# Optimization experiments

Measured on AMD Instinct MI355X. Metric: run time of the kernel, lower is better.

Reference implementation:

```python
import jax, jax.numpy as jnp
import numpy as np

MAP_X = 72; MAP_Y = 72      # global map grid
R = 300                      # number of rooms
MAXS = 8                     # rooms padded to 8x8 (zero-padded occupancy)
E = 32                       # room_embedding_width
N = 128                      # batch
CONV_CH = [64, 128, 256]; KS = [5, 3, 3]
FC = [512, 256]; OUT_W = 512


def setup_inputs() -> dict:
    key = jax.random.key(0)
    ks = jax.random.split(key, 20)
    rng = np.random.default_rng(0)
    widths = rng.integers(1, MAXS + 1, R)
    heights = rng.integers(1, MAXS + 1, R)
    # room_maps[i] is room.map transposed -> [width, height], zero-padded to [MAXS, MAXS]
    rm = np.zeros((R, MAXS, MAXS), np.int32)
    for i in range(R):
        rm[i, :widths[i], :heights[i]] = rng.integers(0, 2, (int(widths[i]), int(heights[i])))
    inp = {}
    # room top-left positions; rooms fit since max size is MAXS
    inp["X"] = jax.random.randint(ks[0], (N, R, 2), 0, MAP_X - MAXS + 1, dtype=jnp.int32)
    inp["room_maps"] = jnp.asarray(rm)
    inp["room_emb"] = jax.random.normal(ks[1], (R, E), jnp.float32)
    cin = [1 + E] + CONV_CH
    for i in range(3):
        k = KS[i]; fan = cin[i] * k * k
        inp[f"conv_w{i}"] = jax.random.normal(ks[2 + 2 * i], (cin[i + 1], cin[i], k, k), jnp.float32) / np.sqrt(fan).astype(np.float32)
        inp[f"conv_b{i}"] = jnp.zeros((cin[i + 1],), jnp.float32)
    fcd = [CONV_CH[-1]] + FC + [OUT_W]
    for i in range(3):
        inp[f"fc_w{i}"] = jax.random.normal(ks[10 + 2 * i], (fcd[i + 1], fcd[i]), jnp.float32) / np.sqrt(fcd[i]).astype(np.float32)
        inp[f"fc_b{i}"] = jnp.zeros((fcd[i + 1],), jnp.float32)
    return inp


def _encode_map(X, room_maps, room_emb):
    # Fused scatter: occupancy channel + embedding channels scattered in one pass.
    rm = room_maps.astype(room_emb.dtype)                    # [R, W, H]
    vals = jnp.concatenate(
        [rm[..., None], rm[..., None] * room_emb[:, None, None, :]], axis=-1
    )                                                        # [R, W, H, 1+E]
    ax = jnp.arange(MAXS)

    def one(pos):  # pos: [R, 2] positions for one batch element
        ix = jnp.broadcast_to(pos[:, 0, None, None] + ax[None, :, None], (R, MAXS, MAXS))
        iy = jnp.broadcast_to(pos[:, 1, None, None] + ax[None, None, :], (R, MAXS, MAXS))
        grid = jnp.zeros((MAP_X, MAP_Y, 1 + E), vals.dtype)
        # padded cells are zero so dropped/duplicate adds are exact
        return grid.at[ix, iy].add(vals, mode="drop")

    out = jax.vmap(one)(X)                                   # [N, MAP_X, MAP_Y, 1+E]
    # torch: transpose(1,3) -> [N, 1+E, MAP_Y, MAP_X]
    return jnp.transpose(out, (0, 3, 2, 1))


def _conv_relu(x, w, b, k):
    p = k // 2
    y = jax.lax.conv_general_dilated(
        x, w, (1, 1), [(p, p), (p, p)], dimension_numbers=("NCHW", "OIHW", "NCHW"))
    return jax.nn.relu(y + b[None, :, None, None])


def _maxpool3s2(x):
    return jax.lax.reduce_window(x, -jnp.inf, jax.lax.max, (1, 1, 3, 3), (1, 1, 2, 2), "VALID")


def reference(X, room_maps, room_emb, conv_w0, conv_b0, conv_w1, conv_b1, conv_w2, conv_b2, fc_w0, fc_b0, fc_w1, fc_b1, fc_w2, fc_b2):
    x = _encode_map(X, room_maps, room_emb)
    for w, b, k in ((conv_w0, conv_b0, KS[0]), (conv_w1, conv_b1, KS[1]), (conv_w2, conv_b2, KS[2])):
        x = _maxpool3s2(_conv_relu(x, w, b, k))
    x = jnp.mean(x, axis=(2, 3))                             # GlobalAvgPool2d
    x = jax.nn.relu(x @ fc_w0.T + fc_b0)
    x = jax.nn.relu(x @ fc_w1.T + fc_b1)
    return x @ fc_w2.T + fc_b2
```

## Files before the change

kernel.cpp:

```cpp
#include <hip/hip_runtime.h>
#include <hip/hip_bf16.h>
#include <cstdint>
#include <cstddef>

#define NB      128
#define RR      300
#define EMB     32

typedef __bf16 bf16x8 __attribute__((ext_vector_type(8)));
typedef float  f32x4  __attribute__((ext_vector_type(4)));
typedef unsigned short ushort8 __attribute__((ext_vector_type(8)));

__device__ __forceinline__ unsigned short f2bf(float f) {
    union { __hip_bfloat16 h; unsigned short u; } c;
    c.h = __float2bfloat16(f);
    return c.u;
}
__device__ __forceinline__ float bf2f(unsigned short u) {
    union { __hip_bfloat16 h; unsigned short u; } c;
    c.u = u;
    return __bfloat162float(c.h);
}

__device__ __forceinline__ void wpack_body(
    const float* __restrict__ w, unsigned short* __restrict__ wPT,
    int COUT, int CIN, int KK, int gpc, int idx, int total)
{
    if (idx >= total) return;
    int kk = idx & 31;
    int t  = idx >> 5;
    int oc = t % COUT;
    int kb = t / COUT;
    int g  = kb * 4 + (kk >> 3);
    int j  = kk & 7;
    int shift = g / gpc;
    int ci    = (g % gpc) * 8 + j;
    float v = (shift < KK && ci < CIN)
        ? w[(size_t)oc * CIN * KK + (size_t)ci * KK + shift] : 0.0f;
    wPT[idx] = f2bf(v);
}

__device__ __forceinline__ void fcT_body(
    const float* __restrict__ w, float* __restrict__ wT, int O, int I, int idx)
{
    if (idx >= O * I) return;
    int i = idx % I, o = idx / I;
    wT[(size_t)i * O + o] = w[idx];
}

__global__ __launch_bounds__(256) void prep_k(
    const int* __restrict__ rm, unsigned long long* __restrict__ masks,
    const float* __restrict__ cw0, unsigned short* __restrict__ WP0,
    const float* __restrict__ cw1, unsigned short* __restrict__ WP1,
    const float* __restrict__ cw2, unsigned short* __restrict__ WP2,
    int* __restrict__ kt0, int* __restrict__ kt1, int* __restrict__ kt2,
    const float* __restrict__ fw0, float* __restrict__ W0T,
    const float* __restrict__ fw1, float* __restrict__ W1T,
    const float* __restrict__ fw2, float* __restrict__ W2T)
{
    const int b = blockIdx.x;
    const int t = threadIdx.x;
    if (b < 2) {
        int r = b * 256 + t;
        if (r < RR) {
            unsigned long long m = 0ull;
            #pragma unroll
            for (int k = 0; k < 64; ++k)
                if (rm[r * 64 + k]) m |= (1ull << k);
            masks[r] = m;
        }
    } else if (b < 258) {
        wpack_body(cw0, WP0, 64, 33, 25, 5, (b - 2) * 256 + t, 32 * 64 * 32);
    } else if (b < 546) {
        wpack_body(cw1, WP1, 128, 64, 9, 8, (b - 258) * 256 + t, 18 * 128 * 32);
    } else if (b < 1698) {
        wpack_body(cw2, WP2, 256, 128, 9, 16, (b - 546) * 256 + t, 36 * 256 * 32);
    } else if (b < 1699) {
        #pragma unroll
        for (int which = 0; which < 3; ++which) {
            int ngr, gpc, K, Wp, CL;
            int* dst;
            if (which == 0)      { ngr = 128; gpc = 5;  K = 5; Wp = 20; CL = 40;  dst = kt0; }
            else if (which == 1) { ngr = 72;  gpc = 8;  K = 3; Wp = 37; CL = 72;  dst = kt1; }
            else                 { ngr = 144; gpc = 16; K = 3; Wp = 19; CL = 136; dst = kt2; }
            if (t < ngr) {
                int shift = t / gpc;
                int off = 0;
                if (shift < K * K) {
                    int ky = shift / K, kx = shift % K;
                    off = (ky * Wp + kx) * CL + (t % gpc) * 8;
                }
                dst[t] = off;
            }
        }
    } else if (b < 2211) {
        fcT_body(fw0, W0T, 512, 256, (b - 1699) * 256 + t);
    } else if (b < 2723) {
        fcT_body(fw1, W1T, 256, 512, (b - 2211) * 256 + t);
    } else {
        fcT_body(fw2, W2T, 512, 256, (b - 2723) * 256 + t);
    }
}

__device__ __forceinline__ void border_body(
    unsigned short* __restrict__ base, int Hp, int Wp, int CPG, int pad,
    int sampleStride, int nborder, int idx, int total)
{
    if (idx >= total) return;
    int c8 = idx % CPG;
    int t  = idx / CPG;
    int bi = t % nborder;
    int nl = t / nborder;

    int topN = pad * Wp;
    int y, x;
    if (bi < topN) {
        y = bi / Wp; x = bi - y * Wp;
    } else if (bi < 2 * topN) {
        int b2 = bi - topN;
        y = Hp - pad + b2 / Wp; x = b2 % Wp;
    } else {
        int mid = bi - 2 * topN;
        int rowlen = 2 * pad;
        y = pad + mid / rowlen;
        int r = mid % rowlen;
        x = r < pad ? r : Wp - pad + (r - pad);
    }
    uint4 z = make_uint4(0, 0, 0, 0);
    *reinterpret_cast<uint4*>(
        &base[((size_t)nl * sampleStride) +
              ((size_t)y * Wp + x) * (CPG * 8) + c8 * 8]) = z;
}

__global__ __launch_bounds__(256) void border2_k(
    unsigned short* __restrict__ bufC, int C_SS, int nb1, int Bc)
{
    int b = blockIdx.x;
    int t = threadIdx.x;
    if (b < nb1) {
        border_body(bufC, 37, 37, 8, 1, C_SS, 144, b * 256 + t, Bc * 144 * 8);
    } else {
        border_body(bufC + 87616, 19, 19, 16, 1, C_SS, 72,
                    (b - nb1) * 256 + t, Bc * 72 * 16);
    }
}

__global__ __launch_bounds__(512) void encode_k(
    const int* __restrict__ X, const unsigned long long* __restrict__ masks,
    const float* __restrict__ emb, unsigned short* __restrict__ G,
    int n0, int sampleStride)
{
    __shared__ float tile[4][72][33];
    __shared__ unsigned s_pos[RR];
    __shared__ unsigned long long s_mask[RR];
    __shared__ unsigned short s_list[320];
    __shared__ float s_emb[64 * 33];
    __shared__ int s_woff[8];
    __shared__ int s_cnt;

    const int nl = blockIdx.x, band = blockIdx.y;
    const int by = band * 4;
    const int n  = n0 + nl;
    const int tid = threadIdx.x;

    float* tf = &tile[0][0][0];
    for (int i = tid; i < 4 * 72 * 33; i += 512) tf[i] = 0.0f;

    const int2* Xp = reinterpret_cast<const int2*>(X);
    bool hot = false;
    if (tid < RR) {
        int2 pos = Xp[n * RR + tid];
        s_pos[tid]  = (unsigned)pos.x | ((unsigned)pos.y << 16);
        s_mask[tid] = masks[tid];
        hot = (pos.y <= by + 3) && (pos.y + 7 >= by);
    }
    unsigned long long bal = __ballot(hot);
    if ((tid & 63) == 0) s_woff[tid >> 6] = (int)__popcll(bal);
    __syncthreads();
    if (tid == 0) {
        int acc = 0;
        #pragma unroll
        for (int w = 0; w < 8; ++w) { int c = s_woff[w]; s_woff[w] = acc; acc += c; }
        s_cnt = acc;
    }
    __syncthreads();
    if (hot) {
        int w = tid >> 6, b = tid & 63;
        unsigned long long before = (b == 0) ? 0ull : (bal & ((1ull << b) - 1ull));
        s_list[s_woff[w] + (int)__popcll(before)] = (unsigned short)tid;
    }
    __syncthreads();

    const int lane = tid & 63;
    const int wvi  = tid >> 6;
    const int dx   = lane >> 3;
    const int c0   = (lane & 7) * 5;
    const int cnt  = s_cnt;

    for (int base = 0; base < cnt; base += 64) {
        int cn = cnt - base; if (cn > 64) cn = 64;
        for (int i = tid; i < cn * 33; i += 512) {
            int hi = i / 33, cc = i - hi * 33;
            int r = s_list[base + hi];
            s_emb[i] = (cc == 0) ? 1.0f : emb[r * EMB + cc - 1];
        }
        __syncthreads();

        int j = wvi;
        for (; j + 8 < cn; j += 16) {
            int rA = s_list[base + j];
            int rB = s_list[base + j + 8];
            unsigned pA = s_pos[rA], pB = s_pos[rB];
            unsigned long long mA = s_mask[rA] >> (dx * 8);
            unsigned long long mB = s_mask[rB] >> (dx * 8);
            int xA = (pA & 0xffff) + dx, yA = pA >> 16;
            int xB = (pB & 0xffff) + dx, yB = pB >> 16;
            float eA[5], eB[5];
            #pragma unroll
            for (int q = 0; q < 5; ++q) {
                eA[q] = (c0 + q < 33) ? s_emb[j * 33 + c0 + q] : 0.0f;
                eB[q] = (c0 + q < 33) ? s_emb[(j + 8) * 33 + c0 + q] : 0.0f;
            }
            #pragma unroll
            for (int dyb = 0; dyb < 4; ++dyb) {
                int dA = by + dyb - yA;
                if ((unsigned)dA < 8u && ((mA >> dA) & 1ull)) {
                    #pragma unroll
                    for (int q = 0; q < 5; ++q)
                        if (c0 + q < 33)
                            atomicAdd(&tile[dyb][xA][c0 + q], eA[q]);
                }
                int dB = by + dyb - yB;
                if ((unsigned)dB < 8u && ((mB >> dB) & 1ull)) {
                    #pragma unroll
                    for (int q = 0; q < 5; ++q)
                        if (c0 + q < 33)
                            atomicAdd(&tile[dyb][xB][c0 + q], eB[q]);
                }
            }
        }
        for (; j < cn; j += 8) {
            int r = s_list[base + j];
            unsigned pxy = s_pos[r];
            int px = pxy & 0xffff, py = pxy >> 16;
            unsigned long long mm = s_mask[r] >> (dx * 8);
            int x = px + dx;
            float ev[5];
            #pragma unroll
            for (int q = 0; q < 5; ++q)
                ev[q] = (c0 + q < 33) ? s_emb[j * 33 + c0 + q] : 0.0f;
            #pragma unroll
            for (int dyb = 0; dyb < 4; ++dyb) {
                int dyr = by + dyb - py;
                if ((unsigned)dyr < 8u && ((mm >> dyr) & 1ull)) {
                    #pragma unroll
                    for (int q = 0; q < 5; ++q)
                        if (c0 + q < 33)
                            atomicAdd(&tile[dyb][x][c0 + q], ev[q]);
                }
            }
        }
        __syncthreads();
    }
    __syncthreads();

    unsigned short* Gn = G + (size_t)nl * sampleStride;
    for (int i = tid; i < 4 * 72 * 10; i += 512) {
        int cc = i % 10;
        int t  = i / 10;
        int x  = t % 72;
        int dyb = t / 72;
        int c0w = cc * 4;
        unsigned short r[4];
        #pragma unroll
        for (int j = 0; j < 4; ++j)
            r[j] = (c0w + j < 33) ? f2bf(tile[dyb][x][c0w + j]) : 0;
        uint2 pk;
        pk.x = (unsigned)r[0] | ((unsigned)r[1] << 16);
        pk.y = (unsigned)r[2] | ((unsigned)r[3] << 16);
        *reinterpret_cast<uint2*>(
            &Gn[((size_t)(by + dyb + 2) * 76 + (x + 2)) * 40 + c0w]) = pk;
    }

    uint2 zz; zz.x = 0; zz.y = 0;
    for (int i = tid; i < 160; i += 512) {
        int cc = i % 10;
        int t  = i / 10;
        int ci = t & 3;
        int dyb = t >> 2;
        int x = ci < 2 ? ci : 72 + ci;
        *reinterpret_cast<uint2*>(
            &Gn[((size_t)(by + dyb + 2) * 76 + x) * 40 + cc * 4]) = zz;
    }
    if (band == 0 || band == 17) {
        int rbase = band == 0 ? 0 : 74;
        for (int i = tid; i < 2 * 76 * 10; i += 512) {
            int cc = i % 10;
            int t  = i / 10;
            int x  = t % 76;
            int r  = t / 76;
            *reinterpret_cast<uint2*>(
                &Gn[((size_t)(rbase + r) * 76 + x) * 40 + cc * 4]) = zz;
        }
    }
}

template<int KSTEPS>
__global__ __launch_bounds__(256, 3) void conv0_tile_k(
    const unsigned short* __restrict__ inP,
    const unsigned short* __restrict__ wPT,
    const int* __restrict__ ktab,
    const float* __restrict__ bias,
    unsigned short* __restrict__ out,
    int inSS, int outSS)
{
    constexpr int CL = 40;
    constexpr int LP = 72;
    __shared__ __align__(16) unsigned short slab[28 * 20 * CL];
    __shared__ int s_kt[KSTEPS * 4];
    unsigned short* s_c = slab;

    const int tid = threadIdx.x;
    const int tl  = blockIdx.x;
    const int nl  = blockIdx.y;
    const int tyi = tl / 5, txi = tl % 5;
    const int y0 = tyi * 24;
    const int x0 = txi < 4 ? txi * 16 : 56;

    const int lane = tid & 63, wv = tid >> 6, frow = lane & 15, fq = lane >> 4;

    if (tid < KSTEPS * 4) s_kt[tid] = ktab[tid];

    const unsigned short* in_n = inP + (size_t)nl * inSS;
    {
        const uint4* src = reinterpret_cast<const uint4*>(in_n);
        uint4* dst = reinterpret_cast<uint4*>(slab);
        #pragma unroll
        for (int it = 0; it < 11; ++it) {
            int q = tid + it * 256;
            if (q < 2800) {
                int r = q / 100, c = q - r * 100;
                dst[q] = src[((y0 + r) * 76 + x0) * 5 + c];
            }
        }
    }

    int ldsb[6];
    #pragma unroll
    for (int mf = 0; mf < 6; ++mf)
        ldsb[mf] = ((mf * 4 + wv) * 20 + frow) * CL;

    const unsigned short* wbase = wPT + (size_t)frow * 32 + fq * 8;

    f32x4 acc[6][4];
    #pragma unroll
    for (int a = 0; a < 6; ++a)
        #pragma unroll
        for (int b = 0; b < 4; ++b) acc[a][b] = (f32x4){0.f, 0.f, 0.f, 0.f};

    __syncthreads();

    #pragma unroll 2
    for (int kb = 0; kb < KSTEPS; ++kb) {
        int go = s_kt[kb * 4 + fq];
        bf16x8 af[6];
        #pragma unroll
        for (int mf = 0; mf < 6; ++mf)
            af[mf] = *reinterpret_cast<const bf16x8*>(&slab[ldsb[mf] + go]);
        const unsigned short* wk = wbase + (size_t)kb * 64 * 32;
        #pragma unroll
        for (int ng = 0; ng < 4; ++ng) {
            bf16x8 bf = *reinterpret_cast<const bf16x8*>(wk + ng * 16 * 32);
            #pragma unroll
            for (int mf = 0; mf < 6; ++mf)
                acc[mf][ng] = __builtin_amdgcn_mfma_f32_16x16x32_bf16(
                    af[mf], bf, acc[mf][ng], 0, 0, 0);
        }
    }

    unsigned short* out_n = out + (size_t)nl * outSS;
    const int erow = tid >> 2, eseg = tid & 3;
    #pragma unroll
    for (int mf = 0; mf < 6; ++mf) {
        __syncthreads();
        #pragma unroll
        for (int ng = 0; ng < 4; ++ng) {
            float bv = bias[ng * 16 + frow];
            #pragma unroll
            for (int j = 0; j < 4; ++j)
                s_c[(wv * 16 + fq * 4 + j) * LP + ng * 16 + frow] =
                    f2bf(fmaxf(acc[mf][ng][j] + bv, 0.0f));
        }
        __syncthreads();
        {
            int ty = mf * 4 + (erow >> 4);
            int tx = erow & 15;
            int pos = (y0 + ty) * 72 + (x0 + tx);
            ushort8 v0 = *reinterpret_cast<const ushort8*>(
                &s_c[erow * LP + eseg * 16]);
            ushort8 v1 = *reinterpret_cast<const ushort8*>(
                &s_c[erow * LP + eseg * 16 + 8]);
            unsigned short* op = out_n + (size_t)pos * 64 + eseg * 16;
            *reinterpret_cast<ushort8*>(op) = v0;
            *reinterpret_cast<ushort8*>(op + 8) = v1;
        }
    }
}

template<int MFRAG, int NG, int KH, int CPG, int CL, int SLAB, int KSTEPS>
__global__ __launch_bounds__(256, 2) void conv_mfma_k(
    const unsigned short* __restrict__ inP,
    const unsigned short* __restrict__ wPT,
    const int* __restrict__ ktab,
    const float* __restrict__ bias,
    unsigned short* __restrict__ out,
    int W, int Wp, int Mtot, int inSS, int outSS, int COUT)
{
    constexpr int Mblk = MFRAG * 64;
    constexpr int NOC  = NG * 16;
    constexpr int SEGS = NOC / 16;
    constexpr int LP   = NOC + 8;
    constexpr int CP   = CPG * 8;
    constexpr int SMEM = (SLAB * 2 > 64 * LP * 2) ? SLAB * 2 : 64 * LP * 2;
    __shared__ __align__(16) char smem[SMEM];
    __shared__ int s_kt[KSTEPS * 4];
    unsigned short* slab = reinterpret_cast<unsigned short*>(smem);
    unsigned short* s_c  = reinterpret_cast<unsigned short*>(smem);

    const int tid  = threadIdx.x;
    const int mb   = blockIdx.x;
    const int ocb  = blockIdx.y;
    const int nl   = blockIdx.z;
    const int lane = tid & 63;
    const int wv   = tid >> 6;
    const int frow = lane & 15;
    const int fq   = lane >> 4;

    if (tid < KSTEPS * 4) s_kt[tid] = ktab[tid];

    const int p0    = mb * Mblk;
    const int y0    = p0 / W;
    const int plast = (p0 + Mblk < Mtot ? p0 + Mblk : Mtot) - 1;
    const int rows  = plast / W - y0 + KH;

    const unsigned short* in_n =
        inP + (size_t)nl * inSS + (size_t)y0 * Wp * CP;
    const int nchunks = rows * Wp * CPG;
    for (int q = tid; q < nchunks; q += 256) {
        int pix = q / CPG, c8 = q - pix * CPG;
        uint4 v = reinterpret_cast<const uint4*>(in_n)[q];
        *reinterpret_cast<uint4*>(&slab[pix * CL + c8 * 8]) = v;
    }

    int ldsb[MFRAG];
    #pragma unroll
    for (int mf = 0; mf < MFRAG; ++mf) {
        int p  = p0 + mf * 64 + wv * 16 + frow;
        int pc = p < Mtot ? p : (Mtot - 1);
        int y  = pc / W;
        int x  = pc - y * W;
        ldsb[mf] = ((y - y0) * Wp + x) * CL;
    }
    const unsigned short* wbase =
        wPT + ((size_t)(ocb * NOC + frow)) * 32 + fq * 8;

    f32x4 acc[MFRAG][NG];
    #pragma unroll
    for (int mf = 0; mf < MFRAG; ++mf)
        #pragma unroll
        for (int ng = 0; ng < NG; ++ng)
            acc[mf][ng] = (f32x4){0.f, 0.f, 0.f, 0.f};

    __syncthreads();

    for (int kb = 0; kb < KSTEPS; ++kb) {
        int go = s_kt[kb * 4 + fq];
        bf16x8 af[MFRAG];
        #pragma unroll
        for (int mf = 0; mf < MFRAG; ++mf)
            af[mf] = *reinterpret_cast<const bf16x8*>(&slab[ldsb[mf] + go]);
        const unsigned short* wk = wbase + (size_t)kb * COUT * 32;
        #pragma unroll
        for (int ng = 0; ng < NG; ++ng) {
            bf16x8 bf = *reinterpret_cast<const bf16x8*>(wk + ng * 16 * 32);
            #pragma unroll
            for (int mf = 0; mf < MFRAG; ++mf)
                acc[mf][ng] = __builtin_amdgcn_mfma_f32_16x16x32_bf16(
                    af[mf], bf, acc[mf][ng], 0, 0, 0);
        }
    }

    unsigned short* out_n = out + (size_t)nl * outSS;
    #pragma unroll
    for (int mf = 0; mf < MFRAG; ++mf) {
        __syncthreads();
        #pragma unroll
        for (int ng = 0; ng < NG; ++ng) {
            float bv = bias[ocb * NOC + ng * 16 + frow];
            #pragma unroll
            for (int j = 0; j < 4; ++j)
                s_c[(wv * 16 + fq * 4 + j) * LP + ng * 16 + frow] =
                    f2bf(fmaxf(acc[mf][ng][j] + bv, 0.0f));
        }
        __syncthreads();
        for (int t = tid; t < 64 * SEGS; t += 256) {
            int row = t / SEGS, seg = t % SEGS;
            int p = p0 + mf * 64 + row;
            if (p < Mtot) {
                ushort8 v0 = *reinterpret_cast<const ushort8*>(
                    &s_c[row * LP + seg * 16]);
                ushort8 v1 = *reinterpret_cast<const ushort8*>(
                    &s_c[row * LP + seg * 16 + 8]);
                unsigned short* op =
                    out_n + (size_t)p * COUT + ocb * NOC + seg * 16;
                *reinterpret_cast<ushort8*>(op) = v0;
                *reinterpret_cast<ushort8*>(op + 8) = v1;
            }
        }
    }
}

__global__ __launch_bounds__(256) void pool_k(
    const unsigned short* __restrict__ in, unsigned short* __restrict__ out,
    int CG, int C, int W, int inSS,
    int HO, int WO, int Wpo, int outSS, int total)
{
    int idx = blockIdx.x * 256 + threadIdx.x;
    if (idx >= total) return;
    int cg = idx % CG;
    int t  = idx / CG;
    int x  = t % WO;
    t /= WO;
    int y  = t % HO;
    int nl = t / HO;

    const unsigned short* pin = in + (size_t)nl * inSS + cg * 8;
    ushort8 mx = {0,0,0,0,0,0,0,0};
    #pragma unroll
    for (int dy = 0; dy < 3; ++dy)
        #pragma unroll
        for (int dx = 0; dx < 3; ++dx) {
            ushort8 v = *reinterpret_cast<const ushort8*>(
                pin + ((size_t)(2 * y + dy) * W + (2 * x + dx)) * C);
            #pragma unroll
            for (int j = 0; j < 8; ++j) mx[j] = v[j] > mx[j] ? v[j] : mx[j];
        }
    *reinterpret_cast<ushort8*>(
        out + (size_t)nl * outSS +
        ((size_t)(y + 1) * Wpo + (x + 1)) * C + cg * 8) = mx;
}

__global__ __launch_bounds__(256) void pool2gap_k(
    const unsigned short* __restrict__ in, float* __restrict__ out,
    int inSS, int n0)
{
    __shared__ float red[4][4][8];
    const int nl = blockIdx.x;
    const int cg = blockIdx.y;
    const int tid = threadIdx.x;
    const int w  = tid >> 2;
    const int cq = tid & 3;
    const int y = w >> 3, x = w & 7;

    const unsigned short* p = in + (size_t)nl * inSS + cg * 32 + cq * 8;
    ushort8 mx = {0,0,0,0,0,0,0,0};
    #pragma unroll
    for (int dy = 0; dy < 3; ++dy)
        #pragma unroll
        for (int dx = 0; dx < 3; ++dx) {
            ushort8 v = *reinterpret_cast<const ushort8*>(
                p + ((size_t)(2 * y + dy) * 17 + (2 * x + dx)) * 256);
            #pragma unroll
            for (int j = 0; j < 8; ++j) mx[j] = v[j] > mx[j] ? v[j] : mx[j];
        }
    float s[8];
    #pragma unroll
    for (int j = 0; j < 8; ++j) s[j] = bf2f(mx[j]);
    #pragma unroll
    for (int m = 4; m < 64; m <<= 1)
        #pragma unroll
        for (int j = 0; j < 8; ++j)
            s[j] += __shfl_xor(s[j], m);
    if ((tid & 63) < 4) {
        #pragma unroll
        for (int j = 0; j < 8; ++j) red[tid >> 6][tid & 3][j] = s[j];
    }
    __syncthreads();
    if (tid < 32) {
        int cq2 = tid >> 3, j = tid & 7;
        float t = red[0][cq2][j] + red[1][cq2][j] + red[2][cq2][j] + red[3][cq2][j];
        out[(size_t)(n0 + nl) * 256 + cg * 32 + cq2 * 8 + j] = t * (1.0f / 64.0f);
    }
}

__global__ __launch_bounds__(256) void fc_fused_k(
    const float* __restrict__ in,
    const float* __restrict__ w0T, const float* __restrict__ b0,
    const float* __restrict__ w1T, const float* __restrict__ b1,
    const float* __restrict__ w2T, const float* __restrict__ b2,
    float* __restrict__ out)
{
    __shared__ float s_in[256], s_h0[512], s_h1[256];
    const int n = blockIdx.x, t = threadIdx.x;
    s_in[t] = in[(size_t)n * 256 + t];
    __syncthreads();
    float a0 = 0.f, a1 = 0.f;
    for (int i = 0; i < 256; ++i) {
        float v = s_in[i];
        a0 += v * w0T[i * 512 + t];
        a1 += v * w0T[i * 512 + t + 256];
    }
    s_h0[t]       = fmaxf(a0 + b0[t], 0.0f);
    s_h0[t + 256] = fmaxf(a1 + b0[t + 256], 0.0f);
    __syncthreads();
    float h = 0.f;
    for (int i = 0; i < 512; ++i) h += s_h0[i] * w1T[i * 256 + t];
    s_h1[t] = fmaxf(h + b1[t], 0.0f);
    __syncthreads();
    a0 = 0.f; a1 = 0.f;
    for (int i = 0; i < 256; ++i) {
        float v = s_h1[i];
        a0 += v * w2T[i * 512 + t];
        a1 += v * w2T[i * 512 + t + 256];
    }
    out[(size_t)n * 512 + t]       = a0 + b2[t];
    out[(size_t)n * 512 + t + 256] = a1 + b2[t + 256];
}

extern "C" void kernel_launch(void* const* d_in, const int* in_sizes, int n_in,
                              void* d_out, int out_size, void* d_ws, size_t ws_size,
                              hipStream_t stream)
{
    const int*   X   = (const int*)d_in[0];
    const int*   rm  = (const int*)d_in[1];
    const float* emb = (const float*)d_in[2];
    const float* cw0 = (const float*)d_in[3];
    const float* cb0 = (const float*)d_in[4];
    const float* cw1 = (const float*)d_in[5];
    const float* cb1 = (const float*)d_in[6];
    const float* cw2 = (const float*)d_in[7];
    const float* cb2 = (const float*)d_in[8];
    const float* fw0 = (const float*)d_in[9];
    const float* fb0 = (const float*)d_in[10];
    const float* fw1 = (const float*)d_in[11];
    const float* fb1 = (const float*)d_in[12];
    const float* fw2 = (const float*)d_in[13];
    const float* fb2 = (const float*)d_in[14];
    float* out = (float*)d_out;

    char* p = (char*)d_ws;
    auto alloc = [&](size_t bytes) -> char* {
        char* r = p; p += (bytes + 255) & ~(size_t)255; return r;
    };
    unsigned short* WP0 = (unsigned short*)alloc((size_t)32 * 64 * 32 * 2);
    unsigned short* WP1 = (unsigned short*)alloc((size_t)18 * 128 * 32 * 2);
    unsigned short* WP2 = (unsigned short*)alloc((size_t)36 * 256 * 32 * 2);
    int* KT0 = (int*)alloc(128 * 4);
    int* KT1 = (int*)alloc(72 * 4);
    int* KT2 = (int*)alloc(144 * 4);
    unsigned long long* MASKS = (unsigned long long*)alloc(RR * 8);
    float* W0T  = (float*)alloc((size_t)256 * 512 * 4);
    float* W1T  = (float*)alloc((size_t)512 * 256 * 4);
    float* W2T  = (float*)alloc((size_t)256 * 512 * 4);
    float* GAPB = (float*)alloc((size_t)NB * 256 * 4);
    size_t fixed_bytes = (size_t)(p - (char*)d_ws);

    const size_t A_FL = 231040, B_FL = 331776, C_FL = 133824;
    const size_t per_sample = (A_FL + B_FL + C_FL) * 2 + 768;
    int Bc = 128;
    while (Bc > 1 && fixed_bytes + (size_t)Bc * per_sample > ws_size) Bc >>= 1;

    unsigned short* bufA = (unsigned short*)alloc((size_t)Bc * A_FL * 2);
    unsigned short* bufC = (unsigned short*)alloc((size_t)Bc * C_FL * 2);
    unsigned short* bufB = (unsigned short*)alloc((size_t)Bc * B_FL * 2);

    prep_k<<<3235, 256, 0, stream>>>(
        rm, MASKS, cw0, WP0, cw1, WP1, cw2, WP2,
        KT0, KT1, KT2, fw0, W0T, fw1, W1T, fw2, W2T);

    for (int n0 = 0; n0 < NB; n0 += Bc) {
        int nbc1 = (Bc * 144 * 8 + 255) / 256;
        int nbc2 = (Bc * 72 * 16 + 255) / 256;
        border2_k<<<nbc1 + nbc2, 256, 0, stream>>>(
            bufC, (int)C_FL, nbc1, Bc);

        encode_k<<<dim3(Bc, 18), 512, 0, stream>>>(X, MASKS, emb, bufA, n0, (int)A_FL);

        conv0_tile_k<32><<<dim3(15, Bc), 256, 0, stream>>>(
            bufA, WP0, KT0, cb0, bufB, (int)A_FL, (int)B_FL);
        pool_k<<<(Bc * 35 * 35 * 8 + 255) / 256, 256, 0, stream>>>(
            bufB, bufC, 8, 64, 72, (int)B_FL,
            35, 35, 37, (int)C_FL, Bc * 35 * 35 * 8);

        conv_mfma_k<4, 8, 3, 8, 72, 29304, 18><<<dim3(5, 1, Bc), 256, 0, stream>>>(
            bufC, WP1, KT1, cb1, bufA, 35, 37,
            1225, (int)C_FL, (int)A_FL, 128);
        pool_k<<<(Bc * 17 * 17 * 16 + 255) / 256, 256, 0, stream>>>(
            bufA, bufC + 87616, 16, 128, 35, (int)A_FL,
            17, 17, 19, (int)C_FL, Bc * 17 * 17 * 16);

        conv_mfma_k<2, 8, 3, 16, 136, 28424, 36><<<dim3(3, 2, Bc), 256, 0, stream>>>(
            bufC + 87616, WP2, KT2, cb2, bufB, 17, 19,
            289, (int)C_FL, (int)B_FL, 256);

        pool2gap_k<<<dim3(Bc, 8), 256, 0, stream>>>(bufB, GAPB, (int)B_FL, n0);
    }

    fc_fused_k<<<NB, 256, 0, stream>>>(GAPB, W0T, fb0, W1T, fb1, W2T, fb2, out);
}
```

Baseline: 487.7 us.

## Fold border zeroing into pool kernels and retile conv2 to one M-tile

Removes the separate border-zeroing kernel launch and has each pool kernel zero the padding border of its output buffer using extra blocks. This saves one launch per chunk. Separately, the third conv's template parameters change from 2 to 5 M-fragments with a larger shared-memory size, so the grid shrinks from 3x2 to 1x2 blocks per sample. The bigger tile cuts repeated weight loads but lowers parallelism and raises LDS use per block.

```diff
diff --git a/kernel.cpp b/kernel.cpp
--- a/kernel.cpp
+++ b/kernel.cpp
@@ -130,19 +130,6 @@
     *reinterpret_cast<uint4*>(
         &base[((size_t)nl * sampleStride) +
               ((size_t)y * Wp + x) * (CPG * 8) + c8 * 8]) = z;
-}
-
-__global__ __launch_bounds__(256) void border2_k(
-    unsigned short* __restrict__ bufC, int C_SS, int nb1, int Bc)
-{
-    int b = blockIdx.x;
-    int t = threadIdx.x;
-    if (b < nb1) {
-        border_body(bufC, 37, 37, 8, 1, C_SS, 144, b * 256 + t, Bc * 144 * 8);
-    } else {
-        border_body(bufC + 87616, 19, 19, 16, 1, C_SS, 72,
-                    (b - nb1) * 256 + t, Bc * 72 * 16);
-    }
 }
 
 __global__ __launch_bounds__(512) void encode_k(
@@ -520,12 +507,20 @@
     }
 }
 
-__global__ __launch_bounds__(256) void pool_k(
+__global__ __launch_bounds__(256) void pool_border_k(
     const unsigned short* __restrict__ in, unsigned short* __restrict__ out,
     int CG, int C, int W, int inSS,
-    int HO, int WO, int Wpo, int outSS, int total)
-{
-    int idx = blockIdx.x * 256 + threadIdx.x;
+    int HO, int WO, int Wpo, int outSS, int total,
+    int npool, int bHp, int bWp, int bCPG, int bpad, int bnborder, int btotal)
+{
+    const int b = blockIdx.x;
+    const int tidx = threadIdx.x;
+    if (b >= npool) {
+        border_body(out, bHp, bWp, bCPG, bpad, outSS, bnborder,
+                    (b - npool) * 256 + tidx, btotal);
+        return;
+    }
+    int idx = b * 256 + tidx;
     if (idx >= total) return;
     int cg = idx % CG;
     int t  = idx / CG;
@@ -679,27 +674,38 @@
         KT0, KT1, KT2, fw0, W0T, fw1, W1T, fw2, W2T);
 
     for (int n0 = 0; n0 < NB; n0 += Bc) {
-        int nbc1 = (Bc * 144 * 8 + 255) / 256;
-        int nbc2 = (Bc * 72 * 16 + 255) / 256;
-        border2_k<<<nbc1 + nbc2, 256, 0, stream>>>(
-            bufC, (int)C_FL, nbc1, Bc);
-
         encode_k<<<dim3(Bc, 18), 512, 0, stream>>>(X, MASKS, emb, bufA, n0, (int)A_FL);
 
         conv0_tile_k<32><<<dim3(15, Bc), 256, 0, stream>>>(
             bufA, WP0, KT0, cb0, bufB, (int)A_FL, (int)B_FL);
-        pool_k<<<(Bc * 35 * 35 * 8 + 255) / 256, 256, 0, stream>>>(
-            bufB, bufC, 8, 64, 72, (int)B_FL,
-            35, 35, 37, (int)C_FL, Bc * 35 * 35 * 8);
+
+        {
+            int total = Bc * 35 * 35 * 8;
+            int npool = (total + 255) / 256;
+            int btotal = Bc * 144 * 8;
+            int nbord = (btotal + 255) / 256;
+            pool_border_k<<<npool + nbord, 256, 0, stream>>>(
+                bufB, bufC, 8, 64, 72, (int)B_FL,
+                35, 35, 37, (int)C_FL, total,
+                npool, 37, 37, 8, 1, 144, btotal);
+        }
 
         conv_mfma_k<4, 8, 3, 8, 72, 29304, 18><<<dim3(5, 1, Bc), 256, 0, stream>>>(
             bufC, WP1, KT1, cb1, bufA, 35, 37,
             1225, (int)C_FL, (int)A_FL, 128);
-        pool_k<<<(Bc * 17 * 17 * 16 + 255) / 256, 256, 0, stream>>>(
-            bufA, bufC + 87616, 16, 128, 35, (int)A_FL,
-            17, 17, 19, (int)C_FL, Bc * 17 * 17 * 16);
-
-        conv_mfma_k<2, 8, 3, 16, 136, 28424, 36><<<dim3(3, 2, Bc), 256, 0, stream>>>(
+
+        {
+            int total = Bc * 17 * 17 * 16;
+            int npool = (total + 255) / 256;
+            int btotal = Bc * 72 * 16;
+            int nbord = (btotal + 255) / 256;
+            pool_border_k<<<npool + nbord, 256, 0, stream>>>(
+                bufA, bufC + 87616, 16, 128, 35, (int)A_FL,
+                17, 17, 19, (int)C_FL, total,
+                npool, 19, 19, 16, 1, 72, btotal);
+        }
+
+        conv_mfma_k<5, 8, 3, 16, 136, 49096, 36><<<dim3(1, 2, Bc), 256, 0, stream>>>(
             bufC + 87616, WP2, KT2, cb2, bufB, 17, 19,
             289, (int)C_FL, (int)B_FL, 256);
 
```

After: 467.3 us. -4.2%, faster.
